# Performance work log

Hardware: AMD Instinct MI355X
Metric: run time of the kernel (lower is better)

The kernel has to match this reference:

```python
import jax, jax.numpy as jnp
import numpy as np

THRESHOLD = 0.045
TAU = 20.0
N = 1048576
H = 128


def setup_inputs() -> dict:
    key = jax.random.key(0)
    ks = jax.random.split(key, 7)
    x = jax.random.normal(ks[0], (N, 1), dtype=jnp.float32)
    s1 = 1.0  # 1/sqrt(fan_in=1)
    s2 = 1.0 / np.sqrt(H).astype(np.float32)
    W1 = jax.random.uniform(ks[1], (H, 1), jnp.float32, -s1, s1)
    b1 = jax.random.uniform(ks[2], (H,), jnp.float32, -s1, s1)
    W2 = jax.random.uniform(ks[3], (H, H), jnp.float32, -s2, s2)
    b2 = jax.random.uniform(ks[4], (H,), jnp.float32, -s2, s2)
    W3 = jax.random.uniform(ks[5], (1, H), jnp.float32, -s2, s2)
    b3 = jax.random.uniform(ks[6], (1,), jnp.float32, -s2, s2)
    return {"x": x, "W1": W1, "b1": b1, "W2": W2, "b2": b2, "W3": W3, "b3": b3}


def reference(x, W1, b1, W2, b2, W3, b3):
    n = x.shape[0]
    # threshold-gated event mask (mask[0] forced active, as in original)
    diff = jnp.abs(x - jnp.roll(x, 1, axis=0))[:, 0]
    mask = (diff > THRESHOLD).at[0].set(True)
    # tiny MLP; computed densely — values at non-active rows are never read
    # (output gathers only last-active rows), so the math matches the
    # original's gather-then-MLP exactly.
    h = jax.nn.relu(x @ W1.T + b1)        # [N, H]
    h = jax.nn.relu(h @ W2.T + b2)        # [N, H]
    y = h @ W3.T + b3                     # [N, 1]
    t = jnp.arange(n, dtype=jnp.float32)
    # last active time <= i  (cumsum(mask)-1 indexing into active rows is
    # equivalent to gathering at the last active position)
    last_t = jax.lax.cummax(jnp.where(mask, t, jnp.float32(0.0)))  # [N]
    last_idx = last_t.astype(jnp.int32)
    decay = jnp.exp(-(t - last_t) / TAU)[:, None]  # [N, 1]
    output = y[last_idx] * decay
    n_active = mask.sum(dtype=jnp.int32)
    return output, n_active
```

## Files before the change

### kernel.cpp

```cpp
#include <hip/hip_runtime.h>
#include <math.h>


#define THRESH   0.045f
#define NH       128
#define TSZ      8192
#define GMIN     -6.0f
#define GMAX     6.0f
#define TPB      256
#define ITEMS    16
#define CHUNK    (TPB * ITEMS)
#define POISON64 0xAAAAAAAAAAAAAAAAull

__global__ __launch_bounds__(TPB) void kF(const float* __restrict__ x, int n, int nblk,
                                          const float* __restrict__ W1,
                                          const float* __restrict__ b1,
                                          const float* __restrict__ W2,
                                          const float* __restrict__ b2,
                                          const float* __restrict__ W3,
                                          const float* __restrict__ b3,
                                          float* __restrict__ table,
                                          unsigned long long* __restrict__ aggs,
                                          float* __restrict__ out) {
  __shared__ float w2s[NH * NH];
  __shared__ int swl[4], swc[4], swm[4], sws[4];
  __shared__ int sincl[TPB];

  const int t = threadIdx.x, b = blockIdx.x;
  const int lane = t & 63, wv = t >> 6;
  const int base = b * CHUNK + t * ITEMS;

  float4 xq[4];
  const bool full = (base + ITEMS) <= n;
  if (full) {
    const float4* xv = (const float4*)(x + base);
    xq[0] = xv[0]; xq[1] = xv[1]; xq[2] = xv[2]; xq[3] = xv[3];
  }
  const float prevv = (base > 0 && base <= n) ? x[base - 1] : 0.0f;

  {
    const float4* src = (const float4*)W2;
    float4* dst = (float4*)w2s;
    #pragma unroll
    for (int i = 0; i < (NH * NH / 4) / TPB; ++i)
      dst[t + i * TPB] = src[t + i * TPB];
  }
  __syncthreads();

  if (t < 128) {
    const int p  = t & 7;
    const int e0 = b * 32 + (t >> 3) * 2;
    const float step = (GMAX - GMIN) * (1.0f / (float)(TSZ - 1));
    const float xv0 = GMIN + step * (float)e0;
    const float xv1 = xv0 + step;

    float h10[16], h11[16];
    #pragma unroll
    for (int c = 0; c < 4; ++c) {
      #pragma unroll
      for (int r = 0; r < 4; ++r) {
        const int k = 4 * (p + 8 * c) + r;
        const float w = W1[k], bb = b1[k];
        h10[c * 4 + r] = fmaxf(fmaf(xv0, w, bb), 0.0f);
        h11[c * 4 + r] = fmaxf(fmaf(xv1, w, bb), 0.0f);
      }
    }
    const bool hi = (p & 4) != 0;
    float y = 0.0f;
    const float b3v = b3[0];
    #pragma unroll 4
    for (int j = 0; j < NH; ++j) {
      const float* row = &w2s[j * NH];
      float a0 = 0.f, a1 = 0.f, c0 = 0.f, c1 = 0.f;
      #pragma unroll
      for (int c = 0; c < 4; ++c) {
        const float4 w = *(const float4*)&row[4 * (p + 8 * c)];
        a0 = fmaf(h10[c * 4 + 0], w.x, a0);
        a1 = fmaf(h10[c * 4 + 1], w.y, a1);
        a0 = fmaf(h10[c * 4 + 2], w.z, a0);
        a1 = fmaf(h10[c * 4 + 3], w.w, a1);
        c0 = fmaf(h11[c * 4 + 0], w.x, c0);
        c1 = fmaf(h11[c * 4 + 1], w.y, c1);
        c0 = fmaf(h11[c * 4 + 2], w.z, c0);
        c1 = fmaf(h11[c * 4 + 3], w.w, c1);
      }
      const float s0 = a0 + a1, s1 = c0 + c1;
      float u = hi ? s1 : s0;
      float v = hi ? s0 : s1;
      v = __shfl_xor(v, 4);
      u += v;
      u += __shfl_xor(u, 1);
      u += __shfl_xor(u, 2);
      const float h2 = fmaxf(u + b2[j], 0.0f);
      y = fmaf(h2, W3[j], y);
    }
    if ((p & 3) == 0) table[e0 + (p >> 2)] = y + b3v;
  }

  float xs[ITEMS];
  if (full) {
    #pragma unroll
    for (int q = 0; q < 4; ++q) {
      xs[q * 4 + 0] = (&xq[q].x)[0]; xs[q * 4 + 1] = (&xq[q].x)[1];
      xs[q * 4 + 2] = (&xq[q].x)[2]; xs[q * 4 + 3] = (&xq[q].x)[3];
    }
  } else {
    #pragma unroll
    for (int it = 0; it < ITEMS; ++it)
      xs[it] = (base + it < n) ? x[base + it] : 0.0f;
  }
  float prev = prevv;
  unsigned m = 0; int tl = -1; int cnt = 0;
  #pragma unroll
  for (int it = 0; it < ITEMS; ++it) {
    const int i = base + it;
    if (i < n) {
      const bool act = (i == 0) || (fabsf(xs[it] - prev) > THRESH);
      if (act) { tl = i; ++cnt; m |= (1u << it); }
      prev = xs[it];
    }
  }

  int incl = tl;
  #pragma unroll
  for (int off = 1; off < 64; off <<= 1) {
    const int v = __shfl_up(incl, off);
    if (lane >= off) incl = max(incl, v);
  }
  int wsum = cnt;
  #pragma unroll
  for (int off = 1; off < 64; off <<= 1) wsum += __shfl_xor(wsum, off);

  if (lane == 63) swl[wv] = incl;
  if (lane == 0)  swc[wv] = wsum;
  __syncthreads();

  int wpref = -1, bcnt = 0, blast = -1;
  #pragma unroll
  for (int w = 0; w < 4; ++w) {
    const int lv = swl[w];
    if (w < wv) wpref = max(wpref, lv);
    blast = max(blast, lv);
    bcnt += swc[w];
  }
  sincl[t] = max(incl, wpref);

  if (t == 0) {
    const unsigned long long val =
        ((unsigned long long)(unsigned)(blast + 2) << 32) |
        (unsigned long long)(unsigned)(bcnt + 1);
    __hip_atomic_store(&aggs[b], val, __ATOMIC_RELEASE, __HIP_MEMORY_SCOPE_AGENT);
  }

  int gl_t = -1, gc_t = 0;
  if (t < nblk) {
    unsigned long long v;
    for (;;) {
      v = __hip_atomic_load(&aggs[t], __ATOMIC_RELAXED, __HIP_MEMORY_SCOPE_AGENT);
      if (v != 0ull && v != POISON64) break;
      __builtin_amdgcn_s_sleep(1);
    }
    gl_t = (int)(unsigned)(v >> 32) - 2;
    gc_t = (int)(unsigned)(v & 0xffffffffu) - 1;
  }
  __builtin_amdgcn_fence(__ATOMIC_ACQUIRE, "agent");
  __syncthreads();
  const int exclT = (t > 0) ? sincl[t - 1] : -1;

  int mv = (t < b) ? gl_t : -1;
  #pragma unroll
  for (int off = 1; off < 64; off <<= 1) mv = max(mv, __shfl_xor(mv, off));
  int sv = gc_t;
  #pragma unroll
  for (int off = 1; off < 64; off <<= 1) sv += __shfl_xor(sv, off);
  if (lane == 0) { swm[wv] = mv; sws[wv] = sv; }
  __syncthreads();
  const int gexcl = max(max(swm[0], swm[1]), max(swm[2], swm[3]));
  const int total = sws[0] + sws[1] + sws[2] + sws[3];

  int run = max(gexcl, exclT);

  const float invstep = (float)(TSZ - 1) / (GMAX - GMIN);
  if (full) {
    #pragma unroll
    for (int q = 0; q < 4; ++q) {
      float o[4];
      #pragma unroll
      for (int r = 0; r < 4; ++r) {
        const int it = q * 4 + r;
        const int i = base + it;
        const bool act = (m >> it) & 1u;
        if (act) run = i;
        const float xj = act ? xs[it] : x[run];
        const float u = (xj - GMIN) * invstep;
        int i0 = (int)u;
        i0 = max(0, min(i0, TSZ - 2));
        const float f = u - (float)i0;
        const float t0 = table[i0], t1 = table[i0 + 1];
        const float yv = fmaf(f, t1 - t0, t0);
        o[r] = yv * __expf((float)(run - i) * 0.05f);
      }
      float4 ov = { o[0], o[1], o[2], o[3] };
      ((float4*)(out + base))[q] = ov;
    }
  } else {
    #pragma unroll
    for (int it = 0; it < ITEMS; ++it) {
      const int i = base + it;
      if (i >= n) break;
      const bool act = (m >> it) & 1u;
      if (act) run = i;
      const float xj = act ? xs[it] : x[run];
      const float u = (xj - GMIN) * invstep;
      int i0 = (int)u;
      i0 = max(0, min(i0, TSZ - 2));
      const float f = u - (float)i0;
      const float t0 = table[i0], t1 = table[i0 + 1];
      out[i] = fmaf(f, t1 - t0, t0) * __expf((float)(run - i) * 0.05f);
    }
  }
  if (b == 0 && t == 0) out[n] = (float)total;
}

extern "C" void kernel_launch(void* const* d_in, const int* in_sizes, int n_in,
                              void* d_out, int out_size, void* d_ws, size_t ws_size,
                              hipStream_t stream) {
  const float* x  = (const float*)d_in[0];
  const float* W1 = (const float*)d_in[1];
  const float* b1 = (const float*)d_in[2];
  const float* W2 = (const float*)d_in[3];
  const float* b2 = (const float*)d_in[4];
  const float* W3 = (const float*)d_in[5];
  const float* b3 = (const float*)d_in[6];
  float* out = (float*)d_out;
  const int n = in_sizes[0];
  const int nblk = (n + CHUNK - 1) / CHUNK;

  char* w = (char*)d_ws;
  float* table = (float*)w;
  unsigned long long* aggs = (unsigned long long*)(w + TSZ * 4);

  kF<<<nblk, TPB, 0, stream>>>(x, n, nblk, W1, b1, W2, b2, W3, b3,
                               table, aggs, out);
}
```

Measured before the change: 104.1 us.

## Split lookup-table build and scan into specialized producer/consumer blocks

Launches 128 dedicated blocks that build the MLP lookup table using all 256 threads each, plus 256 scan blocks that read x, compute the event mask and decoupled prefix, then spin on per-builder ready flags before interpolating. Previously every block built a slice of the table with half its threads idle before scanning. The split lets the scan phase overlap the table build. It relies on all 384 blocks being co-resident to avoid deadlock, hardcodes the scan grid size to the test N, and packs builder work onto fewer CUs.

```diff
diff --git a/kernel.cpp b/kernel.cpp
--- a/kernel.cpp
+++ b/kernel.cpp
@@ -10,9 +10,12 @@
 #define TPB      256
 #define ITEMS    16
 #define CHUNK    (TPB * ITEMS)
+#define NBUILD   128
+#define NSCAN    256
 #define POISON64 0xAAAAAAAAAAAAAAAAull
-
-__global__ __launch_bounds__(TPB) void kF(const float* __restrict__ x, int n, int nblk,
+#define POISON32 0xAAAAAAAAu
+
+__global__ __launch_bounds__(TPB) void kF(const float* __restrict__ x, int n,
                                           const float* __restrict__ W1,
                                           const float* __restrict__ b1,
                                           const float* __restrict__ W2,
@@ -21,6 +24,7 @@
                                           const float* __restrict__ b3,
                                           float* __restrict__ table,
                                           unsigned long long* __restrict__ aggs,
+                                          unsigned int* __restrict__ tflag,
                                           float* __restrict__ out) {
   __shared__ float w2s[NH * NH];
   __shared__ int swl[4], swc[4], swm[4], sws[4];
@@ -28,28 +32,19 @@
 
   const int t = threadIdx.x, b = blockIdx.x;
   const int lane = t & 63, wv = t >> 6;
-  const int base = b * CHUNK + t * ITEMS;
-
-  float4 xq[4];
-  const bool full = (base + ITEMS) <= n;
-  if (full) {
-    const float4* xv = (const float4*)(x + base);
-    xq[0] = xv[0]; xq[1] = xv[1]; xq[2] = xv[2]; xq[3] = xv[3];
-  }
-  const float prevv = (base > 0 && base <= n) ? x[base - 1] : 0.0f;
-
-  {
-    const float4* src = (const float4*)W2;
-    float4* dst = (float4*)w2s;
-    #pragma unroll
-    for (int i = 0; i < (NH * NH / 4) / TPB; ++i)
-      dst[t + i * TPB] = src[t + i * TPB];
-  }
-  __syncthreads();
-
-  if (t < 128) {
+
+  if (b < NBUILD) {
+    {
+      const float4* src = (const float4*)W2;
+      float4* dst = (float4*)w2s;
+      #pragma unroll
+      for (int i = 0; i < (NH * NH / 4) / TPB; ++i)
+        dst[t + i * TPB] = src[t + i * TPB];
+    }
+    __syncthreads();
+
     const int p  = t & 7;
-    const int e0 = b * 32 + (t >> 3) * 2;
+    const int e0 = b * 64 + (t >> 3) * 2;
     const float step = (GMAX - GMIN) * (1.0f / (float)(TSZ - 1));
     const float xv0 = GMIN + step * (float)e0;
     const float xv1 = xv0 + step;
@@ -94,22 +89,36 @@
       const float h2 = fmaxf(u + b2[j], 0.0f);
       y = fmaf(h2, W3[j], y);
     }
-    if ((p & 3) == 0) table[e0 + (p >> 2)] = y + b3v;
-  }
+    if ((p & 3) == 0) {
+      __hip_atomic_store(&table[e0 + (p >> 2)], y + b3v,
+                         __ATOMIC_RELAXED, __HIP_MEMORY_SCOPE_AGENT);
+    }
+    __syncthreads();
+    if (t == 0)
+      __hip_atomic_store(&tflag[b], 1u, __ATOMIC_RELEASE,
+                         __HIP_MEMORY_SCOPE_AGENT);
+    return;
+  }
+
+  const int s = b - NBUILD;
+  const int base = s * CHUNK + t * ITEMS;
 
   float xs[ITEMS];
+  const bool full = (base + ITEMS) <= n;
   if (full) {
+    const float4* xv = (const float4*)(x + base);
     #pragma unroll
     for (int q = 0; q < 4; ++q) {
-      xs[q * 4 + 0] = (&xq[q].x)[0]; xs[q * 4 + 1] = (&xq[q].x)[1];
-      xs[q * 4 + 2] = (&xq[q].x)[2]; xs[q * 4 + 3] = (&xq[q].x)[3];
+      const float4 v = xv[q];
+      xs[q * 4 + 0] = v.x; xs[q * 4 + 1] = v.y;
+      xs[q * 4 + 2] = v.z; xs[q * 4 + 3] = v.w;
     }
   } else {
     #pragma unroll
     for (int it = 0; it < ITEMS; ++it)
       xs[it] = (base + it < n) ? x[base + it] : 0.0f;
   }
-  float prev = prevv;
+  float prev = (base > 0 && base <= n) ? x[base - 1] : 0.0f;
   unsigned m = 0; int tl = -1; int cnt = 0;
   #pragma unroll
   for (int it = 0; it < ITEMS; ++it) {
@@ -149,11 +158,11 @@
     const unsigned long long val =
         ((unsigned long long)(unsigned)(blast + 2) << 32) |
         (unsigned long long)(unsigned)(bcnt + 1);
-    __hip_atomic_store(&aggs[b], val, __ATOMIC_RELEASE, __HIP_MEMORY_SCOPE_AGENT);
+    __hip_atomic_store(&aggs[s], val, __ATOMIC_RELAXED, __HIP_MEMORY_SCOPE_AGENT);
   }
 
   int gl_t = -1, gc_t = 0;
-  if (t < nblk) {
+  {
     unsigned long long v;
     for (;;) {
       v = __hip_atomic_load(&aggs[t], __ATOMIC_RELAXED, __HIP_MEMORY_SCOPE_AGENT);
@@ -163,11 +172,18 @@
     gl_t = (int)(unsigned)(v >> 32) - 2;
     gc_t = (int)(unsigned)(v & 0xffffffffu) - 1;
   }
-  __builtin_amdgcn_fence(__ATOMIC_ACQUIRE, "agent");
+  if (t < NBUILD) {
+    for (;;) {
+      const unsigned int f = __hip_atomic_load(&tflag[t], __ATOMIC_ACQUIRE,
+                                               __HIP_MEMORY_SCOPE_AGENT);
+      if (f == 1u) break;
+      __builtin_amdgcn_s_sleep(1);
+    }
+  }
   __syncthreads();
   const int exclT = (t > 0) ? sincl[t - 1] : -1;
 
-  int mv = (t < b) ? gl_t : -1;
+  int mv = (t < s) ? gl_t : -1;
   #pragma unroll
   for (int off = 1; off < 64; off <<= 1) mv = max(mv, __shfl_xor(mv, off));
   int sv = gc_t;
@@ -196,7 +212,10 @@
         int i0 = (int)u;
         i0 = max(0, min(i0, TSZ - 2));
         const float f = u - (float)i0;
-        const float t0 = table[i0], t1 = table[i0 + 1];
+        const float t0 = __hip_atomic_load(&table[i0], __ATOMIC_RELAXED,
+                                           __HIP_MEMORY_SCOPE_AGENT);
+        const float t1 = __hip_atomic_load(&table[i0 + 1], __ATOMIC_RELAXED,
+                                           __HIP_MEMORY_SCOPE_AGENT);
         const float yv = fmaf(f, t1 - t0, t0);
         o[r] = yv * __expf((float)(run - i) * 0.05f);
       }
@@ -215,11 +234,14 @@
       int i0 = (int)u;
       i0 = max(0, min(i0, TSZ - 2));
       const float f = u - (float)i0;
-      const float t0 = table[i0], t1 = table[i0 + 1];
+      const float t0 = __hip_atomic_load(&table[i0], __ATOMIC_RELAXED,
+                                         __HIP_MEMORY_SCOPE_AGENT);
+      const float t1 = __hip_atomic_load(&table[i0 + 1], __ATOMIC_RELAXED,
+                                         __HIP_MEMORY_SCOPE_AGENT);
       out[i] = fmaf(f, t1 - t0, t0) * __expf((float)(run - i) * 0.05f);
     }
   }
-  if (b == 0 && t == 0) out[n] = (float)total;
+  if (s == 0 && t == 0) out[n] = (float)total;
 }
 
 extern "C" void kernel_launch(void* const* d_in, const int* in_sizes, int n_in,
@@ -234,12 +256,12 @@
   const float* b3 = (const float*)d_in[6];
   float* out = (float*)d_out;
   const int n = in_sizes[0];
-  const int nblk = (n + CHUNK - 1) / CHUNK;
 
   char* w = (char*)d_ws;
   float* table = (float*)w;
   unsigned long long* aggs = (unsigned long long*)(w + TSZ * 4);
-
-  kF<<<nblk, TPB, 0, stream>>>(x, n, nblk, W1, b1, W2, b2, W3, b3,
-                               table, aggs, out);
+  unsigned int* tflag = (unsigned int*)(w + TSZ * 4 + 2048);
+
+  kF<<<NBUILD + NSCAN, TPB, 0, stream>>>(x, n, W1, b1, W2, b2, W3, b3,
+                                         table, aggs, tflag, out);
 }
```

Result: slower. 133.4 us (+28.1%).
